# Kernel optimization log

Hardware: AMD Instinct MI355X
Metric: run time of the kernel (lower is better)

The kernel has to match this reference:

```python
import jax, jax.numpy as jnp
import numpy as np

N, E = 50000, 800000
IN_C, OUT_C, H, EW_DIM = 64, 32, 4, 16
NEG_SLOPE = 0.2


def setup_inputs() -> dict:
    key = jax.random.key(0)
    ks = jax.random.split(key, 10)
    x = jax.random.normal(ks[0], (N, IN_C), dtype=jnp.float32)
    src = jax.random.randint(ks[1], (E,), 0, N)
    dst = jax.random.randint(ks[2], (E,), 0, N)
    edge_index = jnp.stack([src, dst]).astype(jnp.int64)
    edge_weight = jax.random.normal(ks[3], (E, EW_DIM), dtype=jnp.float32)
    # GATConv params: lin weight [IN_C, H*OUT_C], bias [H*OUT_C], att_src/att_dst [H, OUT_C]
    s = 1.0 / np.sqrt(IN_C)
    W = jax.random.uniform(ks[4], (IN_C, H * OUT_C), minval=-s, maxval=s, dtype=jnp.float32)
    b = jnp.zeros((H * OUT_C,), dtype=jnp.float32)
    att_src = jax.random.normal(ks[5], (H, OUT_C), dtype=jnp.float32) * 0.1
    att_dst = jax.random.normal(ks[6], (H, OUT_C), dtype=jnp.float32) * 0.1
    # edge_weight_lin params: [EW_DIM, H], [H]
    se = 1.0 / np.sqrt(EW_DIM)
    Wl = jax.random.uniform(ks[7], (EW_DIM, H), minval=-se, maxval=se, dtype=jnp.float32)
    bl = jax.random.uniform(ks[8], (H,), minval=-se, maxval=se, dtype=jnp.float32)
    return {"x": x, "edge_index": edge_index, "edge_weight": edge_weight,
            "W": W, "b": b, "att_src": att_src, "att_dst": att_dst,
            "Wl": Wl, "bl": bl}


def gate_forward(x, edge_index, edge_weight, W, b, att_src, att_dst, Wl, bl):
    n = x.shape[0]
    h = (x @ W).reshape(n, H, OUT_C)                      # [N,H,C]
    a_src = jnp.einsum('nhc,hc->nh', h, att_src)          # [N,H]
    a_dst = jnp.einsum('nhc,hc->nh', h, att_dst)          # [N,H]
    # per-edge attention logits from edge weights (softmax over heads)
    edge_alpha = jax.nn.softmax(edge_weight @ Wl + bl, axis=1)  # [E,H]
    # add self loops (GATConv default add_self_loops=True, fill_value='mean')
    loop = jnp.arange(n)
    src = jnp.concatenate([edge_index[0], loop])
    dst = jnp.concatenate([edge_index[1], loop])
    loop_alpha = jnp.broadcast_to(edge_alpha.mean(axis=0), (n, H))
    ea = jnp.concatenate([edge_alpha, loop_alpha], axis=0)      # [E+N,H]
    # per-edge logits: gather src/dst contributions + edge term
    alpha = jax.nn.leaky_relu(a_src[src] + a_dst[dst] + ea, NEG_SLOPE)  # [E+N,H]
    # segment softmax grouped by destination node
    amax = jax.ops.segment_max(alpha, dst, num_segments=n)
    ex = jnp.exp(alpha - amax[dst])
    denom = jax.ops.segment_sum(ex, dst, num_segments=n)
    alpha = ex / (denom[dst] + 1e-16)                     # [E+N,H]
    # weighted messages, scatter-add aggregate
    msg = h[src] * alpha[:, :, None]                      # [E+N,H,C]
    out = jax.ops.segment_sum(msg, dst, num_segments=n)   # [N,H,C]
    return out.reshape(n, H * OUT_C) + b


def reference(x, edge_index, edge_weight, W, b, att_src, att_dst, Wl, bl):
    return gate_forward(x, edge_index, edge_weight, W, b, att_src, att_dst, Wl, bl)
```

## Files before the change

### kernel.cpp

```cpp
#include <hip/hip_runtime.h>
#include <math.h>

#define IN_C 64
#define HC 128
#define NHEAD 4
#define EWD 16
#define NEG 0.2f

__device__ __forceinline__ float lrelu(float v) { return v > 0.f ? v : NEG * v; }

__global__ void k_feat(const float* __restrict__ x, const float* __restrict__ W,
                       const float* __restrict__ att_s, const float* __restrict__ att_d,
                       float* __restrict__ h, float* __restrict__ a_src, float* __restrict__ a_dst,
                       int N) {
    __shared__ float Ws[IN_C * HC];
    __shared__ float xs[4][IN_C];
    const int tid = threadIdx.x;
    {
        const float4* W4 = (const float4*)W;
        float4* Ws4 = (float4*)Ws;
#pragma unroll
        for (int i = 0; i < (IN_C * HC / 4) / 128; ++i)
            Ws4[tid + i * 128] = W4[tid + i * 128];
    }
    const float as = att_s[tid];
    const float ad = att_d[tid];
    const int head = tid >> 5;
    for (int base = blockIdx.x * 4; base < N; base += gridDim.x * 4) {
        const int nrows = min(4, N - base);
        __syncthreads();
        if (tid < 64) {
            int r = tid >> 4, q = tid & 15;
            if (r < nrows)
                ((float4*)&xs[r][0])[q] = ((const float4*)(x + (size_t)(base + r) * IN_C))[q];
        }
        __syncthreads();
        for (int r = 0; r < nrows; ++r) {
            float acc = 0.f;
#pragma unroll
            for (int c = 0; c < IN_C; ++c)
                acc = fmaf(xs[r][c], Ws[c * HC + tid], acc);
            const int n = base + r;
            h[(size_t)n * HC + tid] = acc;
            float ps = acc * as, pd = acc * ad;
#pragma unroll
            for (int off = 16; off; off >>= 1) {
                ps += __shfl_xor(ps, off, 32);
                pd += __shfl_xor(pd, off, 32);
            }
            if ((tid & 31) == 0) {
                a_src[n * NHEAD + head] = ps;
                a_dst[n * NHEAD + head] = pd;
            }
        }
    }
}

__global__ void k_count(const int* __restrict__ dst, int* __restrict__ deg, int E) {
    int e = blockIdx.x * 256 + threadIdx.x;
    if (e < E) atomicAdd(&deg[dst[e]], 1);
}

__global__ void k_scan1(const int* __restrict__ deg, int* __restrict__ part, int N) {
    const int b = blockIdx.x, tid = threadIdx.x;
    int base = b * 1024 + tid * 4;
    int s = 0;
#pragma unroll
    for (int k = 0; k < 4; ++k) { int i = base + k; if (i < N) s += deg[i]; }
#pragma unroll
    for (int off = 32; off; off >>= 1) s += __shfl_xor(s, off, 64);
    __shared__ int ls[4];
    if ((tid & 63) == 0) ls[tid >> 6] = s;
    __syncthreads();
    if (tid == 0) part[b] = ls[0] + ls[1] + ls[2] + ls[3];
}

__global__ void k_scan2(int* part, int nb) {
    const int tid = threadIdx.x;
    int orig = (tid < nb) ? part[tid] : 0;
    int v = orig;
#pragma unroll
    for (int off = 1; off < 64; off <<= 1) {
        int t = __shfl_up(v, off, 64);
        if (tid >= off) v += t;
    }
    if (tid < nb) part[tid] = v - orig;
}

__global__ void k_scan3(const int* __restrict__ deg, const int* __restrict__ part,
                        int* __restrict__ rowptr, int* __restrict__ cursor, int N, int E) {
    const int b = blockIdx.x, tid = threadIdx.x;
    int base = b * 1024 + tid * 4;
    int d[4]; int s = 0;
#pragma unroll
    for (int k = 0; k < 4; ++k) { int i = base + k; d[k] = (i < N) ? deg[i] : 0; s += d[k]; }
    int v = s;
#pragma unroll
    for (int off = 1; off < 64; off <<= 1) {
        int t = __shfl_up(v, off, 64);
        if ((tid & 63) >= off) v += t;
    }
    __shared__ int wsum[4];
    if ((tid & 63) == 63) wsum[tid >> 6] = v;
    __syncthreads();
    int waveoff = 0;
    const int w = tid >> 6;
    for (int k = 0; k < w; ++k) waveoff += wsum[k];
    int excl = v - s + waveoff + part[b];
#pragma unroll
    for (int k = 0; k < 4; ++k) {
        int i = base + k;
        if (i < N) { rowptr[i] = excl; cursor[i] = excl; }
        excl += d[k];
    }
    if (b == 0 && tid == 0) rowptr[N] = E;
}

__global__ void k_fill(const int* __restrict__ src, const int* __restrict__ dst,
                       const float* __restrict__ ew, const float* __restrict__ Wl,
                       const float* __restrict__ bl,
                       const float* __restrict__ a_src, const float* __restrict__ a_dst,
                       int* __restrict__ cursor, int* __restrict__ csr_src,
                       float* __restrict__ csr_ex, float* __restrict__ partial, int E) {
    __shared__ float sW[EWD * NHEAD];
    __shared__ float sb[NHEAD];
    __shared__ float sred[4][4];
    const int tid = threadIdx.x;
    if (tid < EWD * NHEAD) sW[tid] = Wl[tid];
    if (tid < NHEAD) sb[tid] = bl[tid];
    __syncthreads();
    float loc[4] = {0.f, 0.f, 0.f, 0.f};
    for (int e = blockIdx.x * 256 + tid; e < E; e += gridDim.x * 256) {
        const float4* w4 = (const float4*)(ew + (size_t)e * EWD);
        float v[4];
#pragma unroll
        for (int hh = 0; hh < 4; ++hh) v[hh] = sb[hh];
#pragma unroll
        for (int q = 0; q < 4; ++q) {
            float4 t = w4[q];
            float tv[4] = {t.x, t.y, t.z, t.w};
#pragma unroll
            for (int k = 0; k < 4; ++k)
#pragma unroll
                for (int hh = 0; hh < 4; ++hh)
                    v[hh] = fmaf(tv[k], sW[(q * 4 + k) * 4 + hh], v[hh]);
        }
        float m = fmaxf(fmaxf(v[0], v[1]), fmaxf(v[2], v[3]));
        float s = 0.f;
#pragma unroll
        for (int hh = 0; hh < 4; ++hh) { v[hh] = __expf(v[hh] - m); s += v[hh]; }
        float inv = 1.f / s;
#pragma unroll
        for (int hh = 0; hh < 4; ++hh) { v[hh] *= inv; loc[hh] += v[hh]; }
        const int sn = src[e], dn = dst[e];
        float4 as = ((const float4*)a_src)[sn];
        float4 ad = ((const float4*)a_dst)[dn];
        float4 ex;
        ex.x = __expf(lrelu(as.x + ad.x + v[0]));
        ex.y = __expf(lrelu(as.y + ad.y + v[1]));
        ex.z = __expf(lrelu(as.z + ad.z + v[2]));
        ex.w = __expf(lrelu(as.w + ad.w + v[3]));
        int slot = atomicAdd(&cursor[dn], 1);
        csr_src[slot] = sn;
        ((float4*)csr_ex)[slot] = ex;
    }
    const int w = tid >> 6;
#pragma unroll
    for (int hh = 0; hh < 4; ++hh) {
        float v = loc[hh];
#pragma unroll
        for (int off = 32; off; off >>= 1) v += __shfl_xor(v, off, 64);
        if ((tid & 63) == 0) sred[w][hh] = v;
    }
    __syncthreads();
    if (tid < 4)
        partial[blockIdx.x * 4 + tid] =
            sred[0][tid] + sred[1][tid] + sred[2][tid] + sred[3][tid];
}

__global__ void k_red(const float* __restrict__ partial, float* __restrict__ asum, int nb) {
    const int tid = threadIdx.x;
    const int w = tid >> 6, lane = tid & 63;
    float s = 0.f;
    for (int b = lane; b < nb; b += 64) s += partial[b * 4 + w];
#pragma unroll
    for (int off = 32; off; off >>= 1) s += __shfl_xor(s, off, 64);
    if (lane == 0) asum[w] = s;
}

__global__ void k_agg(const float* __restrict__ h, const int* __restrict__ rowptr,
                      const int* __restrict__ csr_src, const float* __restrict__ csr_ex,
                      const float* __restrict__ a_src, const float* __restrict__ a_dst,
                      const float* __restrict__ asum, const float* __restrict__ bias,
                      float* __restrict__ out, int N, int E) {
    const int d = blockIdx.x;
    const int tid = threadIdx.x;
    const int head = tid >> 5;
    __shared__ int ssrc[32];
    __shared__ float sex[32][4];
    const int r0 = rowptr[d], r1 = rowptr[d + 1];
    float acc = 0.f, den = 0.f;
    for (int base = r0; base < r1; base += 32) {
        const int cnt = min(32, r1 - base);
        __syncthreads();
        if (tid < cnt) {
            ssrc[tid] = csr_src[base + tid];
            float4 e4 = ((const float4*)csr_ex)[base + tid];
            sex[tid][0] = e4.x; sex[tid][1] = e4.y; sex[tid][2] = e4.z; sex[tid][3] = e4.w;
        }
        __syncthreads();
        for (int k = 0; k < cnt; ++k) {
            const int s = ssrc[k];
            const float ex = sex[k][head];
            acc = fmaf(h[(size_t)s * HC + tid], ex, acc);
            den += ex;
        }
    }
    const float mean = asum[head] * (1.0f / (float)E);
    float l = lrelu(a_src[d * NHEAD + head] + a_dst[d * NHEAD + head] + mean);
    const float exl = __expf(l);
    acc = fmaf(h[(size_t)d * HC + tid], exl, acc);
    den += exl;
    out[(size_t)d * HC + tid] = acc / (den + 1e-16f) + bias[tid];
}

extern "C" void kernel_launch(void* const* d_in, const int* in_sizes, int n_in,
                              void* d_out, int out_size, void* d_ws, size_t ws_size,
                              hipStream_t stream) {
    const float* x     = (const float*)d_in[0];
    const int*   ei    = (const int*)d_in[1];
    const float* ew    = (const float*)d_in[2];
    const float* W     = (const float*)d_in[3];
    const float* bias  = (const float*)d_in[4];
    const float* att_s = (const float*)d_in[5];
    const float* att_d = (const float*)d_in[6];
    const float* Wl    = (const float*)d_in[7];
    const float* bl    = (const float*)d_in[8];
    const int N = in_sizes[0] / IN_C;
    const int E = in_sizes[1] / 2;
    const int* src = ei;
    const int* dst = ei + E;
    float* out = (float*)d_out;

    const int FILL_BLOCKS = 1024;

    float* ws = (float*)d_ws;
    size_t off = 0;
    float* h      = ws + off; off += (size_t)N * HC;
    float* a_src  = ws + off; off += (size_t)N * NHEAD;
    float* a_dst  = ws + off; off += (size_t)N * NHEAD;
    int*   deg    = (int*)(ws + off); off += N;
    float* asum   = ws + off; off += 4;
    int*   part   = (int*)(ws + off); off += 64;
    int*   rowptr = (int*)(ws + off); off += (size_t)N + 4;
    int*   cursor = (int*)(ws + off); off += N;
    int*   csr_src= (int*)(ws + off); off += E;
    float* csr_ex = ws + off; off += (size_t)E * NHEAD;
    float* partial= ws + off; off += (size_t)FILL_BLOCKS * 4;

    hipMemsetAsync(deg, 0, (size_t)N * 4, stream);

    k_feat<<<1024, 128, 0, stream>>>(x, W, att_s, att_d, h, a_src, a_dst, N);
    k_count<<<(E + 255) / 256, 256, 0, stream>>>(dst, deg, E);
    const int nb = (N + 1023) / 1024;
    k_scan1<<<nb, 256, 0, stream>>>(deg, part, N);
    k_scan2<<<1, 64, 0, stream>>>(part, nb);
    k_scan3<<<nb, 256, 0, stream>>>(deg, part, rowptr, cursor, N, E);
    k_fill<<<FILL_BLOCKS, 256, 0, stream>>>(src, dst, ew, Wl, bl, a_src, a_dst,
                                            cursor, csr_src, csr_ex, partial, E);
    k_red<<<1, 256, 0, stream>>>(partial, asum, FILL_BLOCKS);
    k_agg<<<N, 128, 0, stream>>>(h, rowptr, csr_src, csr_ex, a_src, a_dst,
                                 asum, bias, out, N, E);
}
```

Measured before the change: 318.7 us.

## Store edge exps in edge order, CSR holds src/edge-id pairs; unroll aggregation loop

The fill kernel now writes each edge's exp values coalesced in original edge order and scatters only an (src, edge id) int2 into the CSR slot. The aggregation kernel gathers the exp values indirectly through the edge id. The fill kernel goes from a grid-stride loop to one edge per thread with a larger grid, and the feature kernel's grid is doubled. The aggregation inner loop is unrolled by four so several h-row loads are in flight at once. This trades a scattered 16-byte write in fill for an extra indirect gather in aggregation.

```diff
diff --git a/kernel.cpp b/kernel.cpp
--- a/kernel.cpp
+++ b/kernel.cpp
@@ -120,8 +120,8 @@
                        const float* __restrict__ ew, const float* __restrict__ Wl,
                        const float* __restrict__ bl,
                        const float* __restrict__ a_src, const float* __restrict__ a_dst,
-                       int* __restrict__ cursor, int* __restrict__ csr_src,
-                       float* __restrict__ csr_ex, float* __restrict__ partial, int E) {
+                       int* __restrict__ cursor, int2* __restrict__ csr,
+                       float4* __restrict__ ex_edge, float* __restrict__ partial, int E) {
     __shared__ float sW[EWD * NHEAD];
     __shared__ float sb[NHEAD];
     __shared__ float sred[4][4];
@@ -130,7 +130,8 @@
     if (tid < NHEAD) sb[tid] = bl[tid];
     __syncthreads();
     float loc[4] = {0.f, 0.f, 0.f, 0.f};
-    for (int e = blockIdx.x * 256 + tid; e < E; e += gridDim.x * 256) {
+    const int e = blockIdx.x * 256 + tid;
+    if (e < E) {
         const float4* w4 = (const float4*)(ew + (size_t)e * EWD);
         float v[4];
 #pragma unroll
@@ -160,9 +161,9 @@
         ex.y = __expf(lrelu(as.y + ad.y + v[1]));
         ex.z = __expf(lrelu(as.z + ad.z + v[2]));
         ex.w = __expf(lrelu(as.w + ad.w + v[3]));
+        ex_edge[e] = ex;
         int slot = atomicAdd(&cursor[dn], 1);
-        csr_src[slot] = sn;
-        ((float4*)csr_ex)[slot] = ex;
+        csr[slot] = make_int2(sn, e);
     }
     const int w = tid >> 6;
 #pragma unroll
@@ -189,7 +190,7 @@
 }
 
 __global__ void k_agg(const float* __restrict__ h, const int* __restrict__ rowptr,
-                      const int* __restrict__ csr_src, const float* __restrict__ csr_ex,
+                      const int2* __restrict__ csr, const float4* __restrict__ ex_edge,
                       const float* __restrict__ a_src, const float* __restrict__ a_dst,
                       const float* __restrict__ asum, const float* __restrict__ bias,
                       float* __restrict__ out, int N, int E) {
@@ -204,12 +205,27 @@
         const int cnt = min(32, r1 - base);
         __syncthreads();
         if (tid < cnt) {
-            ssrc[tid] = csr_src[base + tid];
-            float4 e4 = ((const float4*)csr_ex)[base + tid];
+            int2 ce = csr[base + tid];
+            ssrc[tid] = ce.x;
+            float4 e4 = ex_edge[ce.y];
             sex[tid][0] = e4.x; sex[tid][1] = e4.y; sex[tid][2] = e4.z; sex[tid][3] = e4.w;
         }
         __syncthreads();
-        for (int k = 0; k < cnt; ++k) {
+        int k = 0;
+        for (; k + 4 <= cnt; k += 4) {
+            const int s0 = ssrc[k], s1 = ssrc[k+1], s2 = ssrc[k+2], s3 = ssrc[k+3];
+            const float e0 = sex[k][head], e1 = sex[k+1][head],
+                        e2 = sex[k+2][head], e3 = sex[k+3][head];
+            const float h0 = h[(size_t)s0 * HC + tid];
+            const float h1 = h[(size_t)s1 * HC + tid];
+            const float h2 = h[(size_t)s2 * HC + tid];
+            const float h3 = h[(size_t)s3 * HC + tid];
+            acc = fmaf(h0, e0, acc); den += e0;
+            acc = fmaf(h1, e1, acc); den += e1;
+            acc = fmaf(h2, e2, acc); den += e2;
+            acc = fmaf(h3, e3, acc); den += e3;
+        }
+        for (; k < cnt; ++k) {
             const int s = ssrc[k];
             const float ex = sex[k][head];
             acc = fmaf(h[(size_t)s * HC + tid], ex, acc);
@@ -242,7 +258,7 @@
     const int* dst = ei + E;
     float* out = (float*)d_out;
 
-    const int FILL_BLOCKS = 1024;
+    const int FILL_BLOCKS = (E + 255) / 256;
 
     float* ws = (float*)d_ws;
     size_t off = 0;
@@ -254,21 +270,21 @@
     int*   part   = (int*)(ws + off); off += 64;
     int*   rowptr = (int*)(ws + off); off += (size_t)N + 4;
     int*   cursor = (int*)(ws + off); off += N;
-    int*   csr_src= (int*)(ws + off); off += E;
-    float* csr_ex = ws + off; off += (size_t)E * NHEAD;
+    int2*  csr    = (int2*)(ws + off); off += (size_t)E * 2;
+    float4* ex_edge = (float4*)(ws + off); off += (size_t)E * 4;
     float* partial= ws + off; off += (size_t)FILL_BLOCKS * 4;
 
     hipMemsetAsync(deg, 0, (size_t)N * 4, stream);
 
-    k_feat<<<1024, 128, 0, stream>>>(x, W, att_s, att_d, h, a_src, a_dst, N);
+    k_feat<<<2048, 128, 0, stream>>>(x, W, att_s, att_d, h, a_src, a_dst, N);
     k_count<<<(E + 255) / 256, 256, 0, stream>>>(dst, deg, E);
     const int nb = (N + 1023) / 1024;
     k_scan1<<<nb, 256, 0, stream>>>(deg, part, N);
     k_scan2<<<1, 64, 0, stream>>>(part, nb);
     k_scan3<<<nb, 256, 0, stream>>>(deg, part, rowptr, cursor, N, E);
     k_fill<<<FILL_BLOCKS, 256, 0, stream>>>(src, dst, ew, Wl, bl, a_src, a_dst,
-                                            cursor, csr_src, csr_ex, partial, E);
+                                            cursor, csr, ex_edge, partial, E);
     k_red<<<1, 256, 0, stream>>>(partial, asum, FILL_BLOCKS);
-    k_agg<<<N, 128, 0, stream>>>(h, rowptr, csr_src, csr_ex, a_src, a_dst,
+    k_agg<<<N, 128, 0, stream>>>(h, rowptr, csr, ex_edge, a_src, a_dst,
                                  asum, bias, out, N, E);
 }
```

New measurement: 332.6 us. 4.4% more time.
